# Performance work log

Measured on AMD Instinct MI355X. Metric: run time of the kernel, lower is better.

## Reference

```python
import jax, jax.numpy as jnp
import numpy as np

N, E, G = 100000, 500000, 1000


def _gat(h_in, src, dst, W, a_s, a_d, b, n):
    # PyG GATConv, heads=1, concat=True, negative_slope=0.2, self-loops already in src/dst
    h = h_in @ W.T                                  # [N, out]
    alpha_src = h @ a_s                             # [N]
    alpha_dst = h @ a_d                             # [N]
    e = jax.nn.leaky_relu(alpha_src[src] + alpha_dst[dst], 0.2)  # [E']
    m = jax.ops.segment_max(e, dst, num_segments=n)
    ex = jnp.exp(e - m[dst])
    den = jax.ops.segment_sum(ex, dst, num_segments=n)
    alpha = ex / den[dst]                           # segment softmax over incoming edges
    out = jax.ops.segment_sum(h[src] * alpha[:, None], dst, num_segments=n)
    return out + b


def _forward(x, edge_index, batch, w1, b1, w2, b2, w3, b3,
             g1w, g1as, g1ad, g1b, g2w, g2as, g2ad, g2b,
             g3w, g3as, g3ad, g3b, g4w, g4as, g4ad, g4b,
             g5w, g5as, g5ad, g5b, lw, lb):
    n = x.shape[0]
    h = jax.nn.relu(x @ w1.T + b1)
    h = jax.nn.relu(h @ w2.T + b2)
    h = jax.nn.relu(h @ w3.T + b3)
    loops = jnp.arange(n)
    src = jnp.concatenate([edge_index[0], loops])   # add self-loops
    dst = jnp.concatenate([edge_index[1], loops])
    h = jax.nn.relu(_gat(h, src, dst, g1w, g1as, g1ad, g1b, n))
    h = jax.nn.relu(_gat(h, src, dst, g2w, g2as, g2ad, g2b, n))
    h = jax.nn.relu(_gat(h, src, dst, g3w, g3as, g3ad, g3b, n))
    h = jax.nn.relu(_gat(h, src, dst, g4w, g4as, g4ad, g4b, n))
    h = jax.nn.relu(_gat(h, src, dst, g5w, g5as, g5ad, g5b, n))
    sums = jax.ops.segment_sum(h, batch, num_segments=G)            # [G,32]
    cnt = jax.ops.segment_sum(jnp.ones((n,), h.dtype), batch, num_segments=G)
    mean = sums / jnp.maximum(cnt, 1.0)[:, None]
    return jax.nn.sigmoid(mean @ lw.T + lb)         # [G,1]


def setup_inputs() -> dict:
    key = jax.random.key(0)
    ks = jax.random.split(key, 24)

    def lin(k, o, i):
        k1, k2 = jax.random.split(k)
        s = 1.0 / np.sqrt(i)
        return (jax.random.uniform(k1, (o, i), jnp.float32, -s, s),
                jax.random.uniform(k2, (o,), jnp.float32, -s, s))

    def gat_p(k, i, o):
        k1, k2, k3 = jax.random.split(k, 3)
        s = 1.0 / np.sqrt(i)
        W = jax.random.uniform(k1, (o, i), jnp.float32, -s, s)
        a_s = jax.random.normal(k2, (o,), jnp.float32) / np.sqrt(o)
        a_d = jax.random.normal(k3, (o,), jnp.float32) / np.sqrt(o)
        return W, a_s, a_d, jnp.zeros((o,), jnp.float32)

    inp = {}
    inp['x'] = jax.random.normal(ks[0], (N, 1), jnp.float32)
    inp['edge_index'] = jax.random.randint(ks[1], (2, E), 0, N)
    inp['batch'] = jnp.sort(jax.random.randint(ks[2], (N,), 0, G))
    inp['w1'], inp['b1'] = lin(ks[3], 16, 1)
    inp['w2'], inp['b2'] = lin(ks[4], 32, 16)
    inp['w3'], inp['b3'] = lin(ks[5], 64, 32)
    dims = [(64, 128), (128, 256), (256, 128), (128, 64), (64, 32)]
    for j, (i, o) in enumerate(dims, start=1):
        W, a_s, a_d, b = gat_p(ks[5 + j], i, o)
        inp[f'g{j}w'], inp[f'g{j}as'], inp[f'g{j}ad'], inp[f'g{j}b'] = W, a_s, a_d, b
    inp['lw'], inp['lb'] = lin(ks[12], 1, 32)
    return inp


def reference(x, edge_index, batch, w1, b1, w2, b2, w3, b3,
              g1w, g1as, g1ad, g1b, g2w, g2as, g2ad, g2b,
              g3w, g3as, g3ad, g3b, g4w, g4as, g4ad, g4b,
              g5w, g5as, g5ad, g5b, lw, lb):
    return _forward(x, edge_index, batch, w1, b1, w2, b2, w3, b3,
                    g1w, g1as, g1ad, g1b, g2w, g2as, g2ad, g2b,
                    g3w, g3as, g3ad, g3b, g4w, g4as, g4ad, g4b,
                    g5w, g5as, g5ad, g5b, lw, lb)
```

## Files before the change

kernel.cpp:

```cpp
#include <hip/hip_runtime.h>
#include <math.h>

typedef __attribute__((ext_vector_type(8))) __bf16 bf16x8;
typedef __attribute__((ext_vector_type(4))) float f32x4;

__device__ inline unsigned short f2bf(float f) {
    unsigned int i = __float_as_uint(f);
    unsigned int r = i + 0x7fffu + ((i >> 16) & 1u);
    return (unsigned short)(r >> 16);
}
__device__ inline float bf2f(unsigned short u) {
    return __uint_as_float(((unsigned int)u) << 16);
}

__global__ __launch_bounds__(256) void prelude_kernel(
    const float* __restrict__ x,
    const float* __restrict__ w1, const float* __restrict__ b1,
    const float* __restrict__ w2, const float* __restrict__ b2,
    const float* __restrict__ w3, const float* __restrict__ b3,
    unsigned short* __restrict__ h0, int n,
    const float* __restrict__ g0, const float* __restrict__ g1, const float* __restrict__ g2,
    const float* __restrict__ g3, const float* __restrict__ g4,
    unsigned short* __restrict__ wbAll,
    const int* __restrict__ batch, int* __restrict__ gstart, int G,
    const int* __restrict__ dst, int* __restrict__ deg, int E,
    int mlpB, int f2bfB, int gsB, int histB,
    const float* __restrict__ as1, const float* __restrict__ ad1,
    float* __restrict__ s1out, float* __restrict__ d1out,
    const float* __restrict__ as2, const float* __restrict__ ad2,
    float* __restrict__ pv2) {
    int b = blockIdx.x;
    int tid = threadIdx.x;
    if (b < mlpB) {
        __shared__ float sw1[16], sb1[16], sw2[32 * 16], sb2[32], sw3[64 * 32], sb3[64];
        __shared__ float ps1[64], pd1[64];
        if (tid < 16) { sw1[tid] = w1[tid]; sb1[tid] = b1[tid]; }
        if (tid < 32) sb2[tid] = b2[tid];
        if (tid < 64) sb3[tid] = b3[tid];
        for (int i = tid; i < 512; i += 256) sw2[i] = w2[i];
        for (int i = tid; i < 2048; i += 256) sw3[i] = w3[i];
        if (tid >= 192) {
            int i = tid - 192;
            float s = 0.f, d = 0.f;
            for (int o = 0; o < 128; o++) {
                float w = g0[o * 64 + i];
                s += as1[o] * w;
                d += ad1[o] * w;
            }
            ps1[i] = s;
            pd1[i] = d;
        }
        __syncthreads();
        int node = b * 256 + tid;
        if (node >= n) return;
        float xv = x[node];
        float t1[16], t2[32];
#pragma unroll
        for (int i = 0; i < 16; i++) t1[i] = fmaxf(sw1[i] * xv + sb1[i], 0.f);
#pragma unroll
        for (int o = 0; o < 32; o++) {
            float a = sb2[o];
#pragma unroll
            for (int i = 0; i < 16; i++) a += sw2[o * 16 + i] * t1[i];
            t2[o] = fmaxf(a, 0.f);
        }
        float sdot = 0.f, ddot = 0.f;
        uint4* gp = (uint4*)(h0 + (size_t)node * 64);
#pragma unroll
        for (int c = 0; c < 8; c++) {
            unsigned int wvec[4];
#pragma unroll
            for (int p = 0; p < 4; p++) {
                int o = c * 8 + p * 2;
                float a0 = sb3[o], a1 = sb3[o + 1];
#pragma unroll
                for (int i = 0; i < 32; i++) {
                    a0 += sw3[o * 32 + i] * t2[i];
                    a1 += sw3[(o + 1) * 32 + i] * t2[i];
                }
                float r0 = fmaxf(a0, 0.f), r1 = fmaxf(a1, 0.f);
                sdot += r0 * ps1[o] + r1 * ps1[o + 1];
                ddot += r0 * pd1[o] + r1 * pd1[o + 1];
                wvec[p] = (unsigned)f2bf(r0) | ((unsigned)f2bf(r1) << 16);
            }
            gp[c] = make_uint4(wvec[0], wvec[1], wvec[2], wvec[3]);
        }
        s1out[node] = sdot;
        d1out[node] = ddot;
    } else if (b < mlpB + f2bfB) {
        int i = (b - mlpB) * 256 + tid;
        float v;
        if (i < 8192) v = g0[i];
        else if (i < 40960) v = g1[i - 8192];
        else if (i < 73728) v = g2[i - 40960];
        else if (i < 81920) v = g3[i - 73728];
        else if (i < 83968) v = g4[i - 81920];
        else return;
        wbAll[i] = f2bf(v);
    } else if (b < mlpB + f2bfB + gsB) {
        int g = (b - mlpB - f2bfB) * 256 + tid;
        if (g > G) return;
        if (g == G) { gstart[G] = n; return; }
        int lo = 0, hi = n;
        while (lo < hi) {
            int mid = (lo + hi) >> 1;
            if (batch[mid] < g) lo = mid + 1;
            else hi = mid;
        }
        gstart[g] = lo;
    } else if (b < mlpB + f2bfB + gsB + histB) {
        int e = (b - mlpB - f2bfB - gsB) * 256 + tid;
        if (e >= E + n) return;
        int d = (e < E) ? dst[e] : (e - E);
        atomicAdd(&deg[d], 1);
    } else {
        if (tid < 128) {
            float s = 0.f;
            for (int o = 0; o < 256; o++) s += as2[o] * g1[o * 128 + tid];
            pv2[tid] = s;
        } else {
            int c = tid - 128;
            float s = 0.f;
            for (int o = 0; o < 256; o++) s += ad2[o] * g1[o * 128 + c];
            pv2[128 + c] = s;
        }
    }
}

template <int BN, int EPI>
__global__ __launch_bounds__(256) void gemm_mfma(
    const unsigned short* __restrict__ A, const unsigned short* __restrict__ Wb,
    unsigned short* __restrict__ Cb,
    const float* __restrict__ avs, const float* __restrict__ avd,
    float* __restrict__ as_, float* __restrict__ ad_,
    const float* __restrict__ bias, int n, int K, int O) {
    constexpr int SN = BN / 32;
    __shared__ unsigned short As[128][72];
    __shared__ unsigned short Ws[BN][72];
    int tid = threadIdx.x;
    int row0 = blockIdx.x * 128, col0 = blockIdx.y * BN;
    int w = tid >> 6, lane = tid & 63;
    int wr = w >> 1, wc = w & 1;
    int quad = lane >> 4, l15 = lane & 15;
    f32x4 acc[4][SN];
#pragma unroll
    for (int mi = 0; mi < 4; mi++)
#pragma unroll
        for (int ni = 0; ni < SN; ni++) acc[mi][ni] = (f32x4){0.f, 0.f, 0.f, 0.f};

    for (int k0 = 0; k0 < K; k0 += 64) {
#pragma unroll
        for (int i = tid; i < 1024; i += 256) {
            int r = i >> 3, c8 = i & 7;
            int gr = row0 + r;
            uint4 v = make_uint4(0u, 0u, 0u, 0u);
            if (gr < n) v = *(const uint4*)(A + (size_t)gr * K + k0 + c8 * 8);
            *(uint4*)&As[r][c8 * 8] = v;
        }
#pragma unroll
        for (int i = tid; i < BN * 8; i += 256) {
            int r = i >> 3, c8 = i & 7;
            uint4 v = *(const uint4*)(Wb + (size_t)(col0 + r) * K + k0 + c8 * 8);
            *(uint4*)&Ws[r][c8 * 8] = v;
        }
        __syncthreads();
#pragma unroll
        for (int kk = 0; kk < 64; kk += 32) {
            bf16x8 bfr[SN];
#pragma unroll
            for (int ni = 0; ni < SN; ni++)
                bfr[ni] = *(const bf16x8*)&Ws[wc * (BN / 2) + ni * 16 + l15][kk + quad * 8];
#pragma unroll
            for (int mi = 0; mi < 4; mi++) {
                bf16x8 afr = *(const bf16x8*)&As[wr * 64 + mi * 16 + l15][kk + quad * 8];
#pragma unroll
                for (int ni = 0; ni < SN; ni++)
                    acc[mi][ni] = __builtin_amdgcn_mfma_f32_16x16x32_bf16(afr, bfr[ni],
                                                                          acc[mi][ni], 0, 0, 0);
            }
        }
        __syncthreads();
    }
    float avsv[SN], avdv[SN], bv[SN];
    int gc[SN];
#pragma unroll
    for (int ni = 0; ni < SN; ni++) {
        gc[ni] = col0 + wc * (BN / 2) + ni * 16 + l15;
        if constexpr (EPI != 2) {
            avsv[ni] = avs[gc[ni]];
            avdv[ni] = avd[gc[ni]];
        }
        if constexpr (EPI >= 1) bv[ni] = bias[gc[ni]];
    }
#pragma unroll
    for (int mi = 0; mi < 4; mi++) {
        int gm0 = row0 + wr * 64 + mi * 16 + quad * 4;
        float ps[4] = {0.f, 0.f, 0.f, 0.f}, pd[4] = {0.f, 0.f, 0.f, 0.f};
#pragma unroll
        for (int ni = 0; ni < SN; ni++) {
#pragma unroll
            for (int r = 0; r < 4; r++) {
                float d = acc[mi][ni][r];
                if constexpr (EPI >= 1) d = fmaxf(d + bv[ni], 0.f);
                int gm = gm0 + r;
                if (gm < n) Cb[(size_t)gm * O + gc[ni]] = f2bf(d);
                if constexpr (EPI != 2) {
                    ps[r] += d * avsv[ni];
                    pd[r] += d * avdv[ni];
                }
            }
        }
        if constexpr (EPI != 2) {
#pragma unroll
            for (int r = 0; r < 4; r++) {
#pragma unroll
                for (int m = 1; m <= 8; m <<= 1) {
                    ps[r] += __shfl_xor(ps[r], m);
                    pd[r] += __shfl_xor(pd[r], m);
                }
            }
            if (l15 == 0) {
#pragma unroll
                for (int r = 0; r < 4; r++) {
                    int gm = gm0 + r;
                    if (gm < n) {
                        atomicAdd(&as_[gm], ps[r]);
                        atomicAdd(&ad_[gm], pd[r]);
                    }
                }
            }
        }
    }
}

__global__ void scan_block_sums(const int* __restrict__ deg, int* __restrict__ bsums, int n) {
    __shared__ int sdata[256];
    int tid = threadIdx.x;
    int base = blockIdx.x * 1024 + tid * 4;
    int s = 0;
    for (int i = 0; i < 4; i++) {
        int g = base + i;
        if (g < n) s += deg[g];
    }
    sdata[tid] = s;
    __syncthreads();
    for (int off = 128; off > 0; off >>= 1) {
        if (tid < off) sdata[tid] += sdata[tid + off];
        __syncthreads();
    }
    if (tid == 0) bsums[blockIdx.x] = sdata[0];
}

__global__ void scan_write(const int* __restrict__ deg, const int* __restrict__ bsums,
                           int* __restrict__ rowptr, int* __restrict__ cursor, int n, int nb) {
    __shared__ int sdata[256];
    int tid = threadIdx.x;
    sdata[tid] = (tid < blockIdx.x && tid < nb) ? bsums[tid] : 0;
    __syncthreads();
    for (int off = 128; off > 0; off >>= 1) {
        if (tid < off) sdata[tid] += sdata[tid + off];
        __syncthreads();
    }
    int base = sdata[0];
    __syncthreads();
    int gbase = blockIdx.x * 1024 + tid * 4;
    int v[4];
    int s = 0;
    for (int i = 0; i < 4; i++) {
        int g = gbase + i;
        v[i] = (g < n) ? deg[g] : 0;
        s += v[i];
    }
    sdata[tid] = s;
    __syncthreads();
    for (int off = 1; off < 256; off <<= 1) {
        int t = (tid >= off) ? sdata[tid - off] : 0;
        __syncthreads();
        sdata[tid] += t;
        __syncthreads();
    }
    int excl = sdata[tid] - s + base;
    for (int i = 0; i < 4; i++) {
        int g = gbase + i;
        if (g < n) { rowptr[g] = excl; cursor[g] = excl; }
        excl += v[i];
    }
    if (blockIdx.x == gridDim.x - 1 && tid == 255) rowptr[n] = base + sdata[255];
}

__global__ void scatter_kernel(const int* __restrict__ esrc_in, const int* __restrict__ edst_in,
                               int* __restrict__ cursor, int* __restrict__ esrc, int E, int n) {
    int e = blockIdx.x * 256 + threadIdx.x;
    if (e >= E + n) return;
    int s, d;
    if (e < E) { s = esrc_in[e]; d = edst_in[e]; }
    else { s = e - E; d = e - E; }
    int pos = atomicAdd(&cursor[d], 1);
    esrc[pos] = s;
}

template <int O, bool BIASRELU>
__global__ __launch_bounds__(256) void gat_aggregate(
    const unsigned short* __restrict__ hl, const float* __restrict__ as_,
    const float* __restrict__ ad_, const int* __restrict__ rowptr,
    const int* __restrict__ esrc, const float* __restrict__ bias,
    unsigned short* __restrict__ hout, int n, float* __restrict__ zeroBuf, int zeroCnt) {
    int gtid = blockIdx.x * 256 + threadIdx.x;
    if (gtid < zeroCnt) zeroBuf[gtid] = 0.f;
    constexpr int C8 = O / 8;
    constexpr int EPW = 64 / C8;
    int v = blockIdx.x * 4 + (threadIdx.x >> 6);
    int lane = threadIdx.x & 63;
    if (v >= n) return;
    int beg = rowptr[v], end = rowptr[v + 1];
    int deg = end - beg;
    float adv = ad_[v];
    int sub = lane / C8;
    int c = lane % C8;
    float acc[8] = {0.f, 0.f, 0.f, 0.f, 0.f, 0.f, 0.f, 0.f};
    if (deg <= 64) {
        int sreg = v;
        float e = -1e30f;
        if (lane < deg) {
            sreg = esrc[beg + lane];
            float t = as_[sreg] + adv;
            e = (t > 0.f) ? t : 0.2f * t;
        }
        float m = e;
#pragma unroll
        for (int o = 32; o > 0; o >>= 1) m = fmaxf(m, __shfl_xor(m, o));
        float ex = (lane < deg) ? __expf(e - m) : 0.f;
        float sum = ex;
#pragma unroll
        for (int o = 32; o > 0; o >>= 1) sum += __shfl_xor(sum, o);
        float alpha_r = ex / sum;
        for (int j0 = 0; j0 < deg; j0 += EPW) {
            int idx = j0 + sub;
            int cidx = (idx < deg) ? idx : 0;
            float alpha = __shfl(alpha_r, cidx);
            int s2 = __shfl(sreg, cidx);
            if (idx >= deg) alpha = 0.f;
            uint4 raw = ((const uint4*)(hl + (size_t)s2 * O))[c];
            acc[0] += alpha * __uint_as_float(raw.x << 16);
            acc[1] += alpha * __uint_as_float(raw.x & 0xffff0000u);
            acc[2] += alpha * __uint_as_float(raw.y << 16);
            acc[3] += alpha * __uint_as_float(raw.y & 0xffff0000u);
            acc[4] += alpha * __uint_as_float(raw.z << 16);
            acc[5] += alpha * __uint_as_float(raw.z & 0xffff0000u);
            acc[6] += alpha * __uint_as_float(raw.w << 16);
            acc[7] += alpha * __uint_as_float(raw.w & 0xffff0000u);
        }
    } else {
        float mymax = -1e30f;
        for (int j = beg + lane; j < end; j += 64) {
            float e = as_[esrc[j]] + adv;
            e = (e > 0.f) ? e : 0.2f * e;
            mymax = fmaxf(mymax, e);
        }
#pragma unroll
        for (int o = 32; o > 0; o >>= 1) mymax = fmaxf(mymax, __shfl_xor(mymax, o));
        float mysum = 0.f;
        for (int j = beg + lane; j < end; j += 64) {
            float e = as_[esrc[j]] + adv;
            e = (e > 0.f) ? e : 0.2f * e;
            mysum += __expf(e - mymax);
        }
#pragma unroll
        for (int o = 32; o > 0; o >>= 1) mysum += __shfl_xor(mysum, o);
        float invden = 1.f / mysum;
        for (int j0 = beg; j0 < end; j0 += EPW) {
            int j = j0 + sub;
            bool valid = j < end;
            int s = valid ? esrc[j] : v;
            float e = as_[s] + adv;
            e = (e > 0.f) ? e : 0.2f * e;
            float alpha = valid ? __expf(e - mymax) * invden : 0.f;
            uint4 raw = ((const uint4*)(hl + (size_t)s * O))[c];
            acc[0] += alpha * __uint_as_float(raw.x << 16);
            acc[1] += alpha * __uint_as_float(raw.x & 0xffff0000u);
            acc[2] += alpha * __uint_as_float(raw.y << 16);
            acc[3] += alpha * __uint_as_float(raw.y & 0xffff0000u);
            acc[4] += alpha * __uint_as_float(raw.z << 16);
            acc[5] += alpha * __uint_as_float(raw.z & 0xffff0000u);
            acc[6] += alpha * __uint_as_float(raw.w << 16);
            acc[7] += alpha * __uint_as_float(raw.w & 0xffff0000u);
        }
    }
#pragma unroll
    for (int o = C8; o < 64; o <<= 1)
#pragma unroll
        for (int k = 0; k < 8; k++) acc[k] += __shfl_xor(acc[k], o);
    if (sub == 0) {
        unsigned short ov[8];
#pragma unroll
        for (int k = 0; k < 8; k++) {
            float val = acc[k];
            if constexpr (BIASRELU) val = fmaxf(val + bias[c * 8 + k], 0.f);
            ov[k] = f2bf(val);
        }
        uint4 packed;
        packed.x = (unsigned)ov[0] | ((unsigned)ov[1] << 16);
        packed.y = (unsigned)ov[2] | ((unsigned)ov[3] << 16);
        packed.z = (unsigned)ov[4] | ((unsigned)ov[5] << 16);
        packed.w = (unsigned)ov[6] | ((unsigned)ov[7] << 16);
        ((uint4*)(hout + (size_t)v * O))[c] = packed;
    }
}

__global__ __launch_bounds__(256) void pool_final_kernel(
    const unsigned short* __restrict__ h, const int* __restrict__ start,
    const float* __restrict__ lw, const float* __restrict__ lb,
    float* __restrict__ out, int G) {
    __shared__ float red[8][33];
    int g = blockIdx.x;
    if (g >= G) return;
    int beg = start[g], end = start[g + 1];
    int tid = threadIdx.x;
    int nodeLane = tid >> 5, f = tid & 31;
    float acc = 0.f;
    for (int v = beg + nodeLane; v < end; v += 8)
        acc += bf2f(h[(size_t)v * 32 + f]);
    red[nodeLane][f] = acc;
    __syncthreads();
    if (tid < 32) {
        float s = 0.f;
#pragma unroll
        for (int i = 0; i < 8; i++) s += red[i][f];
        float inv = 1.f / fmaxf((float)(end - beg), 1.f);
        float val = s * inv * lw[f];
#pragma unroll
        for (int o = 16; o > 0; o >>= 1) val += __shfl_xor(val, o);
        if (f == 0) out[g] = 1.f / (1.f + __expf(-(val + lb[0])));
    }
}

extern "C" void kernel_launch(void* const* d_in, const int* in_sizes, int n_in,
                              void* d_out, int out_size, void* d_ws, size_t ws_size,
                              hipStream_t stream) {
    const float* x = (const float*)d_in[0];
    const int* ei = (const int*)d_in[1];
    const int* batch = (const int*)d_in[2];
    const float* w1 = (const float*)d_in[3];
    const float* b1 = (const float*)d_in[4];
    const float* w2 = (const float*)d_in[5];
    const float* b2 = (const float*)d_in[6];
    const float* w3 = (const float*)d_in[7];
    const float* b3 = (const float*)d_in[8];
    const float* gw[5];
    const float* gas[5];
    const float* gad[5];
    const float* gb[5];
    for (int l = 0; l < 5; l++) {
        gw[l] = (const float*)d_in[9 + l * 4 + 0];
        gas[l] = (const float*)d_in[9 + l * 4 + 1];
        gad[l] = (const float*)d_in[9 + l * 4 + 2];
        gb[l] = (const float*)d_in[9 + l * 4 + 3];
    }
    const float* lw = (const float*)d_in[29];
    const float* lb = (const float*)d_in[30];
    float* out = (float*)d_out;

    int N = in_sizes[0];
    int E = in_sizes[1] / 2;
    int G = out_size;
    int Etot = E + N;

    char* ws = (char*)d_ws;
    size_t off = 0;
    auto alloc = [&](size_t bytes) -> void* {
        void* p = ws + off;
        off = (off + bytes + 255) & ~(size_t)255;
        return p;
    };
    unsigned short* actA = (unsigned short*)alloc((size_t)N * 256 * 2);
    unsigned short* actB = (unsigned short*)alloc((size_t)N * 256 * 2);
    char* zblock = (char*)alloc((size_t)N * 20);
    float* sd2 = (float*)zblock;
    float* sd3 = sd2 + (size_t)N * 2;
    int* deg = (int*)(zblock + (size_t)N * 16);
    float* sd1 = (float*)alloc((size_t)N * 2 * 4);
    float* pv2 = (float*)alloc(256 * 4);
    int* rowptr = (int*)alloc((size_t)(N + 1) * 4);
    int* cursor = (int*)alloc((size_t)(N + 1) * 4);
    int* esrc = (int*)alloc((size_t)Etot * 4);
    int* bsums = (int*)alloc(4096);
    int* gstart = (int*)alloc((size_t)(G + 1) * 4);
    unsigned short* wbAll = (unsigned short*)alloc((size_t)83968 * 2);
    const int woff[5] = {0, 8192, 40960, 73728, 81920};
    unsigned short* wb[5];
    for (int l = 0; l < 5; l++) wb[l] = wbAll + woff[l];
    (void)ws_size;
    (void)n_in;

    hipMemsetAsync(zblock, 0, (size_t)N * 20, stream);

    int mlpB = (N + 255) / 256;
    int f2bfB = (83968 + 255) / 256;
    int gsB = (G + 1 + 255) / 256;
    int histB = (Etot + 255) / 256;
    prelude_kernel<<<mlpB + f2bfB + gsB + histB + 1, 256, 0, stream>>>(
        x, w1, b1, w2, b2, w3, b3, actA, N, gw[0], gw[1], gw[2], gw[3], gw[4], wbAll, batch,
        gstart, G, ei + E, deg, E, mlpB, f2bfB, gsB, histB,
        gas[0], gad[0], sd1, sd1 + N, gas[1], gad[1], pv2);

    int nb = (N + 1023) / 1024;
    scan_block_sums<<<nb, 256, 0, stream>>>(deg, bsums, N);
    scan_write<<<nb, 256, 0, stream>>>(deg, bsums, rowptr, cursor, N, nb);
    scatter_kernel<<<(Etot + 255) / 256, 256, 0, stream>>>(ei, ei + E, cursor, esrc, E, N);

    int aggBlocks = (N + 3) / 4;
    int gx = (N + 127) / 128;

    gat_aggregate<64, false><<<aggBlocks, 256, 0, stream>>>(
        actA, sd1, sd1 + N, rowptr, esrc, nullptr, actB, N, nullptr, 0);
    {
        dim3 grid(gx, 2);
        gemm_mfma<64, 1><<<grid, 256, 0, stream>>>(actB, wb[0], actA, pv2, pv2 + 128, sd2,
                                                   sd2 + N, gb[0], N, 64, 128);
    }

    gat_aggregate<128, false><<<aggBlocks, 256, 0, stream>>>(
        actA, sd2, sd2 + N, rowptr, esrc, nullptr, actB, N, sd1, 2 * N);
    {
        dim3 grid(gx, 4);
        gemm_mfma<64, 2><<<grid, 256, 0, stream>>>(actB, wb[1], actA, nullptr, nullptr,
                                                   nullptr, nullptr, gb[1], N, 128, 256);
    }

    {
        dim3 grid(gx, 2);
        gemm_mfma<64, 0><<<grid, 256, 0, stream>>>(actA, wb[2], actB, gas[2], gad[2], sd3,
                                                   sd3 + N, nullptr, N, 256, 128);
    }
    gat_aggregate<128, true><<<aggBlocks, 256, 0, stream>>>(
        actB, sd3, sd3 + N, rowptr, esrc, gb[2], actA, N, sd2, 2 * N);

    {
        dim3 grid(gx, 1);
        gemm_mfma<64, 0><<<grid, 256, 0, stream>>>(actA, wb[3], actB, gas[3], gad[3], sd1,
                                                   sd1 + N, nullptr, N, 128, 64);
    }
    gat_aggregate<64, true><<<aggBlocks, 256, 0, stream>>>(
        actB, sd1, sd1 + N, rowptr, esrc, gb[3], actA, N, nullptr, 0);

    {
        dim3 grid(gx, 1);
        gemm_mfma<32, 0><<<grid, 256, 0, stream>>>(actA, wb[4], actB, gas[4], gad[4], sd2,
                                                   sd2 + N, nullptr, N, 64, 32);
    }
    gat_aggregate<32, true><<<aggBlocks, 256, 0, stream>>>(
        actB, sd2, sd2 + N, rowptr, esrc, gb[4], actA, N, nullptr, 0);

    pool_final_kernel<<<G, 256, 0, stream>>>(actA, gstart, lw, lb, out, G);
}
```

Before: 560.0 us.

## Assign 16-lane groups per node in GAT aggregation instead of full wavefront

The aggregation kernel now maps each destination node to a 16-lane sub-group, so one 64-lane wavefront handles four nodes instead of one. The grid shrinks to match, and the shuffle reductions for softmax and feature accumulation run over 16 lanes. With an average in-degree of about six, a full wavefront per node left most lanes idle; this is meant to recover that lost occupancy and memory parallelism. The trade-off is fewer edges processed in parallel per node for wide feature dimensions, and the fast path now only covers degrees of 16 or less. Feature widths above 128 would break the 16-lane layout.

```diff
diff --git a/kernel.cpp b/kernel.cpp
--- a/kernel.cpp
+++ b/kernel.cpp
@@ -308,37 +308,39 @@
     int gtid = blockIdx.x * 256 + threadIdx.x;
     if (gtid < zeroCnt) zeroBuf[gtid] = 0.f;
     constexpr int C8 = O / 8;
-    constexpr int EPW = 64 / C8;
-    int v = blockIdx.x * 4 + (threadIdx.x >> 6);
-    int lane = threadIdx.x & 63;
+    constexpr int EPP = 16 / C8;
+    int tid = threadIdx.x;
+    int v = blockIdx.x * 16 + (tid >> 4);
+    int l = tid & 15;
+    int gbase = tid & 48;
     if (v >= n) return;
     int beg = rowptr[v], end = rowptr[v + 1];
     int deg = end - beg;
     float adv = ad_[v];
-    int sub = lane / C8;
-    int c = lane % C8;
+    int sub = l / C8;
+    int c = l % C8;
     float acc[8] = {0.f, 0.f, 0.f, 0.f, 0.f, 0.f, 0.f, 0.f};
-    if (deg <= 64) {
+    if (deg <= 16) {
         int sreg = v;
         float e = -1e30f;
-        if (lane < deg) {
-            sreg = esrc[beg + lane];
+        if (l < deg) {
+            sreg = esrc[beg + l];
             float t = as_[sreg] + adv;
             e = (t > 0.f) ? t : 0.2f * t;
         }
         float m = e;
 #pragma unroll
-        for (int o = 32; o > 0; o >>= 1) m = fmaxf(m, __shfl_xor(m, o));
-        float ex = (lane < deg) ? __expf(e - m) : 0.f;
+        for (int o = 8; o > 0; o >>= 1) m = fmaxf(m, __shfl_xor(m, o));
+        float ex = (l < deg) ? __expf(e - m) : 0.f;
         float sum = ex;
 #pragma unroll
-        for (int o = 32; o > 0; o >>= 1) sum += __shfl_xor(sum, o);
+        for (int o = 8; o > 0; o >>= 1) sum += __shfl_xor(sum, o);
         float alpha_r = ex / sum;
-        for (int j0 = 0; j0 < deg; j0 += EPW) {
+        for (int j0 = 0; j0 < deg; j0 += EPP) {
             int idx = j0 + sub;
             int cidx = (idx < deg) ? idx : 0;
-            float alpha = __shfl(alpha_r, cidx);
-            int s2 = __shfl(sreg, cidx);
+            float alpha = __shfl(alpha_r, gbase + cidx);
+            int s2 = __shfl(sreg, gbase + cidx);
             if (idx >= deg) alpha = 0.f;
             uint4 raw = ((const uint4*)(hl + (size_t)s2 * O))[c];
             acc[0] += alpha * __uint_as_float(raw.x << 16);
@@ -352,23 +354,23 @@
         }
     } else {
         float mymax = -1e30f;
-        for (int j = beg + lane; j < end; j += 64) {
+        for (int j = beg + l; j < end; j += 16) {
             float e = as_[esrc[j]] + adv;
             e = (e > 0.f) ? e : 0.2f * e;
             mymax = fmaxf(mymax, e);
         }
 #pragma unroll
-        for (int o = 32; o > 0; o >>= 1) mymax = fmaxf(mymax, __shfl_xor(mymax, o));
+        for (int o = 8; o > 0; o >>= 1) mymax = fmaxf(mymax, __shfl_xor(mymax, o));
         float mysum = 0.f;
-        for (int j = beg + lane; j < end; j += 64) {
+        for (int j = beg + l; j < end; j += 16) {
             float e = as_[esrc[j]] + adv;
             e = (e > 0.f) ? e : 0.2f * e;
             mysum += __expf(e - mymax);
         }
 #pragma unroll
-        for (int o = 32; o > 0; o >>= 1) mysum += __shfl_xor(mysum, o);
+        for (int o = 8; o > 0; o >>= 1) mysum += __shfl_xor(mysum, o);
         float invden = 1.f / mysum;
-        for (int j0 = beg; j0 < end; j0 += EPW) {
+        for (int j0 = beg; j0 < end; j0 += EPP) {
             int j = j0 + sub;
             bool valid = j < end;
             int s = valid ? esrc[j] : v;
@@ -387,10 +389,10 @@
         }
     }
 #pragma unroll
-    for (int o = C8; o < 64; o <<= 1)
+    for (int o = C8; o < 16; o <<= 1)
 #pragma unroll
         for (int k = 0; k < 8; k++) acc[k] += __shfl_xor(acc[k], o);
-    if (sub == 0) {
+    if (l < C8) {
         unsigned short ov[8];
 #pragma unroll
         for (int k = 0; k < 8; k++) {
@@ -508,7 +510,7 @@
     scan_write<<<nb, 256, 0, stream>>>(deg, bsums, rowptr, cursor, N, nb);
     scatter_kernel<<<(Etot + 255) / 256, 256, 0, stream>>>(ei, ei + E, cursor, esrc, E, N);
 
-    int aggBlocks = (N + 3) / 4;
+    int aggBlocks = (N + 15) / 16;
     int gx = (N + 127) / 128;
 
     gat_aggregate<64, false><<<aggBlocks, 256, 0, stream>>>(
```

New measurement: 462.1 us. 17.5% less time.
